# Optimization experiments

Hardware: AMD Instinct MI355X
Metric: run time of the kernel (lower is better)

Reference implementation:

```python
import jax, jax.numpy as jnp
import numpy as np

D_MODEL = 1024
NUM_HEADS = 16
D_IN = 1024

def setup_inputs() -> dict:
    key = jax.random.key(0)
    ks = jax.random.split(key, 5)
    scale = 1.0 / np.sqrt(D_IN)
    return {
        "in_features": jax.random.normal(ks[0], (4, 2048, D_IN), dtype=jnp.float32),
        "q_weight": jax.random.normal(ks[1], (D_MODEL, D_IN), dtype=jnp.float32) * scale,
        "k_weight": jax.random.normal(ks[2], (D_MODEL, D_IN), dtype=jnp.float32) * scale,
        "v_weight": jax.random.normal(ks[3], (D_MODEL, D_IN), dtype=jnp.float32) * scale,
        "o_weight": jax.random.normal(ks[4], (D_MODEL, D_MODEL), dtype=jnp.float32) * scale,
    }

def reference(in_features, q_weight, k_weight, v_weight, o_weight):
    batch, seq_len, _ = in_features.shape
    d_head = D_MODEL // NUM_HEADS
    # QKV projections (Linear with no bias: x @ W^T)
    q = jnp.einsum('bsi,di->bsd', in_features, q_weight)
    k = jnp.einsum('bsi,di->bsd', in_features, k_weight)
    v = jnp.einsum('bsi,di->bsd', in_features, v_weight)
    # split heads -> [b, h, s, d_head]
    q = q.reshape(batch, seq_len, NUM_HEADS, d_head).transpose(0, 2, 1, 3)
    k = k.reshape(batch, seq_len, NUM_HEADS, d_head).transpose(0, 2, 1, 3)
    v = v.reshape(batch, seq_len, NUM_HEADS, d_head).transpose(0, 2, 1, 3)
    # scaled dot-product attention (scale by per-head dim, as in SelfAttention)
    scores = jnp.einsum('bhqd,bhkd->bhqk', q, k) / jnp.sqrt(jnp.float32(d_head))
    probs = jax.nn.softmax(scores, axis=-1)
    ctx = jnp.einsum('bhqk,bhkd->bhqd', probs, v)
    # merge heads -> [b, s, d_model]
    ctx = ctx.transpose(0, 2, 1, 3).reshape(batch, seq_len, D_MODEL)
    # output projection
    return jnp.einsum('bsd,md->bsm', ctx, o_weight)
```

## Files before the change

kernel.cpp:

```cpp
#include <hip/hip_runtime.h>

typedef _Float16 half8 __attribute__((ext_vector_type(8)));
typedef _Float16 half4v __attribute__((ext_vector_type(4)));
typedef __fp16 fp16x2 __attribute__((ext_vector_type(2)));
typedef float f32x4 __attribute__((ext_vector_type(4)));
typedef float f32x16 __attribute__((ext_vector_type(16)));

__device__ __forceinline__ void gload_lds16(const _Float16* g, _Float16* l) {
    __builtin_amdgcn_global_load_lds(
        (const __attribute__((address_space(1))) void*)g,
        (__attribute__((address_space(3))) void*)l,
        16, 0, 0);
}

__global__ void cvt4_f32_f16(const float* __restrict__ s0, const float* __restrict__ s1,
                             const float* __restrict__ s2, const float* __restrict__ s3,
                             _Float16* __restrict__ dst) {
    int i = blockIdx.x * blockDim.x + threadIdx.x;
    int wsel = blockIdx.y;
    const float* src = (wsel == 0) ? s0 : (wsel == 1) ? s1 : (wsel == 2) ? s2 : s3;
    f32x4 v = ((const f32x4*)src)[i];
    half4v h;
    h[0] = (_Float16)v[0]; h[1] = (_Float16)v[1];
    h[2] = (_Float16)v[2]; h[3] = (_Float16)v[3];
    ((half4v*)(dst + (size_t)wsel * 1048576))[i] = h;
}

__global__ __launch_bounds__(256, 2)
void gemm_qkv(const float* __restrict__ X,
              const _Float16* __restrict__ Wbase,
              _Float16* __restrict__ outbase)
{
    __shared__ _Float16 As[2][4096];
    __shared__ _Float16 Bs[2][4096];

    const int tid  = threadIdx.x;
    const int lane = tid & 63;
    const int w    = tid >> 6;
    const int wr   = w >> 1, wc = w & 1;
    const int lr   = lane & 15, lg = lane >> 4;
    const int brow = blockIdx.x * 128;
    const int bcol = blockIdx.y * 128;
    const int mat  = blockIdx.z;

    const float*    Ap = X + (size_t)brow * 1024;
    const _Float16* Bp = Wbase + (size_t)mat * (1024u * 1024u) + (size_t)bcol * 1024;

    const int srw = tid >> 2;
    const int sch = tid & 3;
    const int rsw = (srw >> 1) & 3;
    const int bso = ((sch ^ rsw) << 3);
    const int aw0 = srw * 32        + ((sch ^ rsw) << 3);
    const int aw1 = (64 + srw) * 32 + ((sch ^ rsw) << 3);

    auto stageB = [&](int buf, int kt) {
        gload_lds16(Bp + (size_t)srw * 1024 + kt * 32 + bso,        &Bs[buf][w * 512]);
        gload_lds16(Bp + (size_t)(64 + srw) * 1024 + kt * 32 + bso, &Bs[buf][2048 + w * 512]);
    };

    f32x4 pa0, pa1, pa2, pa3;
    auto loadA = [&](int kt) {
        const float* p0 = Ap + (size_t)srw * 1024 + kt * 32 + sch * 8;
        const float* p1 = Ap + (size_t)(64 + srw) * 1024 + kt * 32 + sch * 8;
        pa0 = *(const f32x4*)p0;  pa1 = *(const f32x4*)(p0 + 4);
        pa2 = *(const f32x4*)p1;  pa3 = *(const f32x4*)(p1 + 4);
    };
    auto writeA = [&](int buf) {
        half8 h0, h1;
#pragma unroll
        for (int e = 0; e < 4; ++e) {
            h0[e]     = (_Float16)pa0[e];
            h0[4 + e] = (_Float16)pa1[e];
            h1[e]     = (_Float16)pa2[e];
            h1[4 + e] = (_Float16)pa3[e];
        }
        *(half8*)&As[buf][aw0] = h0;
        *(half8*)&As[buf][aw1] = h1;
    };

    f32x4 acc[4][4] = {};
    const int swz = ((lg ^ ((lr >> 1) & 3)) << 3);

    loadA(0);
    stageB(0, 0);
    writeA(0);
    loadA(1);
    __syncthreads();

    for (int t = 0; t < 32; ++t) {
        const int cur = t & 1;
        if (t < 31) {
            writeA(cur ^ 1);
            stageB(cur ^ 1, t + 1);
        }
        if (t < 30) loadA(t + 2);
        half8 af[4], bf[4];
#pragma unroll
        for (int mi = 0; mi < 4; ++mi)
            af[mi] = *(const half8*)&As[cur][(wr * 64 + mi * 16 + lr) * 32 + swz];
#pragma unroll
        for (int ni = 0; ni < 4; ++ni)
            bf[ni] = *(const half8*)&Bs[cur][(wc * 64 + ni * 16 + lr) * 32 + swz];
        __builtin_amdgcn_s_setprio(1);
#pragma unroll
        for (int mi = 0; mi < 4; ++mi)
#pragma unroll
            for (int ni = 0; ni < 4; ++ni)
                acc[mi][ni] = __builtin_amdgcn_mfma_f32_16x16x32_f16(af[mi], bf[ni], acc[mi][ni], 0, 0, 0);
        __builtin_amdgcn_s_setprio(0);
        __syncthreads();
    }

    _Float16* outp = outbase + (size_t)mat * (8192u * 1024u);
    if (mat == 2) {
        _Float16* Ts = &As[0][0];
#pragma unroll
        for (int p = 0; p < 2; ++p) {
            __syncthreads();
            if (wc == p) {
#pragma unroll
                for (int mi = 0; mi < 4; ++mi)
#pragma unroll
                    for (int ni = 0; ni < 4; ++ni) {
                        int drow = ni * 16 + lr;
                        int s0   = wr * 64 + mi * 16 + lg * 4;
                        half4v o;
#pragma unroll
                        for (int r = 0; r < 4; ++r) o[r] = (_Float16)acc[mi][ni][r];
                        int byteoff = drow * 256 + s0 * 2;
                        byteoff ^= (drow & 7) << 4;
                        *(half4v*)((char*)Ts + byteoff) = o;
                    }
            }
            __syncthreads();
            {
                int row   = tid >> 2;
                int cbase = (tid & 3) * 4;
                int gd = bcol + p * 64 + row;
                int h = gd >> 6, dd = gd & 63;
                int b = brow >> 11, sseq = brow & 2047;
                _Float16* gout = outp + (((size_t)b * 16 + h) * 64 + dd) * 2048 + sseq;
#pragma unroll
                for (int j = 0; j < 4; ++j) {
                    int c  = cbase + j;
                    int lc = c ^ (row & 7);
                    half8 v = *(const half8*)&Ts[row * 128 + lc * 8];
                    *(half8*)&gout[c * 8] = v;
                }
            }
        }
    } else {
        const float scale = (mat == 0) ? 0.18033688f : 1.0f;
#pragma unroll
        for (int mi = 0; mi < 4; ++mi)
#pragma unroll
            for (int ni = 0; ni < 4; ++ni)
#pragma unroll
                for (int r = 0; r < 4; ++r) {
                    int row = brow + wr * 64 + mi * 16 + lg * 4 + r;
                    int col = bcol + wc * 64 + ni * 16 + lr;
                    int b = row >> 11, s = row & 2047;
                    int h = col >> 6,  d = col & 63;
                    outp[(((size_t)b * 16 + h) * 2048 + s) * 64 + d] =
                        (_Float16)(acc[mi][ni][r] * scale);
                }
    }
}

__global__ __launch_bounds__(256, 2)
void gemm_o(const _Float16* __restrict__ A,
            const _Float16* __restrict__ Wbase,
            float* __restrict__ outp)
{
    __shared__ _Float16 lds[32768];
    _Float16* Asb = lds;
    _Float16* Bsb = lds + 16384;

    const int tid  = threadIdx.x;
    const int lane = tid & 63;
    const int w    = tid >> 6;
    const int wr   = w >> 1, wc = w & 1;
    const int lr   = lane & 15, lg = lane >> 4;
    const int brow = blockIdx.x * 128;
    const int bcol = blockIdx.y * 128;

    const _Float16* Ap = A + (size_t)brow * 1024;
    const _Float16* Bp = Wbase + (size_t)bcol * 1024;

    const int srw  = tid >> 2;
    const int sch  = tid & 3;
    const int soff = ((sch ^ ((srw >> 1) & 3)) << 3);

    auto stage = [&](int buf, int kt) {
#pragma unroll
        for (int i = 0; i < 2; ++i) {
            const int ra = i * 64 + srw;
            gload_lds16(Ap + (size_t)ra * 1024 + kt * 32 + soff,
                        Asb + buf * 4096 + i * 2048 + w * 512);
            gload_lds16(Bp + (size_t)ra * 1024 + kt * 32 + soff,
                        Bsb + buf * 4096 + i * 2048 + w * 512);
        }
    };

    f32x4 acc[4][4] = {};
    const int swz = ((lg ^ ((lr >> 1) & 3)) << 3);

    stage(0, 0);
    stage(1, 1);
    asm volatile("s_waitcnt vmcnt(4)" ::: "memory");
    __builtin_amdgcn_s_barrier();
    __builtin_amdgcn_sched_barrier(0);

    for (int t = 0; t < 32; ++t) {
        if (t < 30) stage((t + 2) & 3, t + 2);
        const _Float16* Ab = Asb + (t & 3) * 4096;
        const _Float16* Bb = Bsb + (t & 3) * 4096;
        half8 af[4], bf[4];
#pragma unroll
        for (int mi = 0; mi < 4; ++mi)
            af[mi] = *(const half8*)&Ab[(wr * 64 + mi * 16 + lr) * 32 + swz];
#pragma unroll
        for (int ni = 0; ni < 4; ++ni)
            bf[ni] = *(const half8*)&Bb[(wc * 64 + ni * 16 + lr) * 32 + swz];
        __builtin_amdgcn_s_setprio(1);
#pragma unroll
        for (int mi = 0; mi < 4; ++mi)
#pragma unroll
            for (int ni = 0; ni < 4; ++ni)
                acc[mi][ni] = __builtin_amdgcn_mfma_f32_16x16x32_f16(af[mi], bf[ni], acc[mi][ni], 0, 0, 0);
        __builtin_amdgcn_s_setprio(0);
        if (t < 30)       { asm volatile("s_waitcnt vmcnt(4)" ::: "memory"); }
        else if (t == 30) { asm volatile("s_waitcnt vmcnt(0)" ::: "memory"); }
        if (t < 31) {
            __builtin_amdgcn_s_barrier();
            __builtin_amdgcn_sched_barrier(0);
        }
    }

#pragma unroll
    for (int mi = 0; mi < 4; ++mi)
#pragma unroll
        for (int ni = 0; ni < 4; ++ni)
#pragma unroll
            for (int r = 0; r < 4; ++r) {
                int row = brow + wr * 64 + mi * 16 + lg * 4 + r;
                int col = bcol + wc * 64 + ni * 16 + lr;
                outp[(size_t)row * 1024 + col] = acc[mi][ni][r];
            }
}

#define M_FIX 10.0f
__global__ __launch_bounds__(256, 4)
void attn_kernel(const _Float16* __restrict__ Q,
                 const _Float16* __restrict__ Kx,
                 const _Float16* __restrict__ Vt,
                 _Float16* __restrict__ Ctx)
{
    __shared__ _Float16 Ks[2][64 * 72];
    __shared__ _Float16 Vs[2][64 * 72];

    const int tid = threadIdx.x, lane = tid & 63, w = tid >> 6;
    const int l31 = lane & 31, hi = lane >> 5;

    const int wg = blockIdx.x;
    const int j = ((wg & 7) << 7) + (wg >> 3);
    const int bh = j >> 4, qblk = j & 15;

    const _Float16* Qp  = Q  + ((size_t)bh * 2048 + qblk * 128) * 64;
    const _Float16* Kp  = Kx + (size_t)bh * 2048 * 64;
    const _Float16* Vtp = Vt + (size_t)bh * 64 * 2048;

    half8 qf[4];
#pragma unroll
    for (int ks = 0; ks < 4; ++ks)
        qf[ks] = *(const half8*)(Qp + (size_t)(w * 32 + l31) * 64 + ks * 16 + hi * 8);

    const int srow = tid >> 3;
    const int scol = (tid & 7) * 8;
    const _Float16* Kg0 = Kp  + (size_t)srow * 64   + scol;
    const _Float16* Vg0 = Vtp + (size_t)srow * 2048 + scol;
    const int ldso = srow * 72 + scol;

    const fp16x2 ones2 = {(__fp16)1.0f, (__fp16)1.0f};

    f32x16 cacc[2] = {};
    float l0 = 0.f, l1 = 0.f;

    half8 kr0, kr1, vr0, vr1;
    kr0 = *(const half8*)(Kg0);
    kr1 = *(const half8*)(Kg0 + 2048);
    vr0 = *(const half8*)(Vg0);
    vr1 = *(const half8*)(Vg0 + 32 * 2048);
    *(half8*)&Ks[0][ldso]           = kr0;
    *(half8*)&Ks[0][ldso + 32 * 72] = kr1;
    *(half8*)&Vs[0][ldso]           = vr0;
    *(half8*)&Vs[0][ldso + 32 * 72] = vr1;
    __syncthreads();

    for (int t = 0; t < 32; ++t) {
        const int cur = t & 1;
        if (t < 31) {
            kr0 = *(const half8*)(Kg0 + (size_t)(t + 1) * 4096);
            kr1 = *(const half8*)(Kg0 + (size_t)(t + 1) * 4096 + 2048);
        }

        f32x16 sf[2];
        __builtin_amdgcn_s_setprio(1);
#pragma unroll
        for (int kt = 0; kt < 2; ++kt) {
            f32x16 z;
#pragma unroll
            for (int r = 0; r < 16; ++r) z[r] = -M_FIX;
#pragma unroll
            for (int ks = 0; ks < 4; ++ks) {
                half8 kf = *(const half8*)&Ks[cur][(kt * 32 + l31) * 72 + ks * 16 + hi * 8];
                z = __builtin_amdgcn_mfma_f32_32x32x16_f16(kf, qf[ks], z, 0, 0, 0);
            }
            sf[kt] = z;
        }
        __builtin_amdgcn_s_setprio(0);

        if (t < 31) {
            *(half8*)&Ks[cur ^ 1][ldso]           = kr0;
            *(half8*)&Ks[cur ^ 1][ldso + 32 * 72] = kr1;
            vr0 = *(const half8*)(Vg0 + (t + 1) * 64);
            vr1 = *(const half8*)(Vg0 + (t + 1) * 64 + 32 * 2048);
        }

        half8 bf[4];
#pragma unroll
        for (int kt = 0; kt < 2; ++kt) {
#pragma unroll
            for (int r = 0; r < 16; ++r)
                sf[kt][r] = __builtin_amdgcn_exp2f(sf[kt][r]);

            unsigned uq[4][2];
#pragma unroll
            for (int qd = 0; qd < 4; ++qd)
#pragma unroll
                for (int w2 = 0; w2 < 2; ++w2)
                    uq[qd][w2] = __builtin_bit_cast(unsigned,
                        __builtin_amdgcn_cvt_pkrtz(sf[kt][4 * qd + 2 * w2],
                                                   sf[kt][4 * qd + 2 * w2 + 1]));

#pragma unroll
            for (int k1 = 0; k1 < 2; ++k1) {
                union { half8 h; unsigned u[4]; } bu;
#pragma unroll
                for (int w2 = 0; w2 < 2; ++w2) {
                    unsigned a = uq[2 * k1][w2];
                    unsigned b = uq[2 * k1 + 1][w2];
                    asm("v_permlane32_swap_b32 %0, %1" : "+v"(a), "+v"(b));
                    bu.u[w2]     = a;
                    bu.u[2 + w2] = b;
                }
                l0 = __builtin_amdgcn_fdot2(__builtin_bit_cast(fp16x2, bu.u[0]), ones2, l0, false);
                l1 = __builtin_amdgcn_fdot2(__builtin_bit_cast(fp16x2, bu.u[1]), ones2, l1, false);
                l0 = __builtin_amdgcn_fdot2(__builtin_bit_cast(fp16x2, bu.u[2]), ones2, l0, false);
                l1 = __builtin_amdgcn_fdot2(__builtin_bit_cast(fp16x2, bu.u[3]), ones2, l1, false);
                bf[kt * 2 + k1] = bu.h;
            }
        }

        __builtin_amdgcn_s_setprio(1);
#pragma unroll
        for (int dt = 0; dt < 2; ++dt)
#pragma unroll
            for (int ks = 0; ks < 4; ++ks) {
                half8 vf = *(const half8*)&Vs[cur][(dt * 32 + l31) * 72 + ks * 16 + hi * 8];
                cacc[dt] = __builtin_amdgcn_mfma_f32_32x32x16_f16(vf, bf[ks], cacc[dt], 0, 0, 0);
            }
        __builtin_amdgcn_s_setprio(0);

        if (t < 31) {
            *(half8*)&Vs[cur ^ 1][ldso]           = vr0;
            *(half8*)&Vs[cur ^ 1][ldso + 32 * 72] = vr1;
        }
        __syncthreads();
    }

    float l = l0 + l1;
    const float inv = 1.0f / (l + __shfl_xor(l, 32, 64));
    const int s = qblk * 128 + w * 32 + l31;
    _Float16* Cp = Ctx + ((size_t)(bh >> 4) * 2048 + s) * 1024 + (bh & 15) * 64;
#pragma unroll
    for (int dt = 0; dt < 2; ++dt)
#pragma unroll
        for (int qd = 0; qd < 4; ++qd) {
            half4v o;
#pragma unroll
            for (int j2 = 0; j2 < 4; ++j2) o[j2] = (_Float16)(cacc[dt][4 * qd + j2] * inv);
            *(half4v*)&Cp[dt * 32 + qd * 8 + hi * 4] = o;
        }
}

extern "C" void kernel_launch(void* const* d_in, const int* in_sizes, int n_in,
                              void* d_out, int out_size, void* d_ws, size_t ws_size,
                              hipStream_t stream)
{
    const float* X  = (const float*)d_in[0];
    const float* Wq = (const float*)d_in[1];
    const float* Wk = (const float*)d_in[2];
    const float* Wv = (const float*)d_in[3];
    const float* Wo = (const float*)d_in[4];

    if (ws_size < (size_t)(8 + 4 + 24) * 1024 * 1024 * 2) return;
    _Float16* Ctx = (_Float16*)d_ws;
    _Float16* Wh  = Ctx + (size_t)8 * 1024 * 1024;
    _Float16* QKV = Wh + (size_t)4 * 1024 * 1024;

    cvt4_f32_f16<<<dim3(1024, 4), 256, 0, stream>>>(Wq, Wk, Wv, Wo, Wh);

    gemm_qkv<<<dim3(64, 8, 3), 256, 0, stream>>>(X, Wh, QKV);

    attn_kernel<<<1024, 256, 0, stream>>>(QKV, QKV + 8388608, QKV + 16777216, Ctx);

    gemm_o<<<dim3(64, 8), 256, 0, stream>>>(Ctx, Wh + 3145728, (float*)d_out);
}
```

Measured before the change: 191.1 us.

## Stage attention K/V tiles via direct global-to-LDS loads with XOR swizzle

Replaces the register-staged K/V prefetch (global load into registers, then LDS store) in the attention kernel with buffer global_load_lds 16-byte direct copies into a double-buffered LDS tile. The padded 72-stride layout becomes an unpadded 64-stride layout with an XOR chunk swizzle to avoid bank conflicts on the MFMA fragment reads. This frees VGPRs and removes the explicit LDS store instructions. It relies on the single per-iteration barrier to cover completion of the asynchronous LDS writes, and the swizzle must match the per-wave contiguous destination layout.

```diff
diff --git a/kernel.cpp b/kernel.cpp
--- a/kernel.cpp
+++ b/kernel.cpp
@@ -256,8 +256,8 @@
                  const _Float16* __restrict__ Vt,
                  _Float16* __restrict__ Ctx)
 {
-    __shared__ _Float16 Ks[2][64 * 72];
-    __shared__ _Float16 Vs[2][64 * 72];
+    __shared__ _Float16 Ks[2][4096];
+    __shared__ _Float16 Vs[2][4096];
 
     const int tid = threadIdx.x, lane = tid & 63, w = tid >> 6;
     const int l31 = lane & 31, hi = lane >> 5;
@@ -276,33 +276,29 @@
         qf[ks] = *(const half8*)(Qp + (size_t)(w * 32 + l31) * 64 + ks * 16 + hi * 8);
 
     const int srow = tid >> 3;
-    const int scol = (tid & 7) * 8;
-    const _Float16* Kg0 = Kp  + (size_t)srow * 64   + scol;
-    const _Float16* Vg0 = Vtp + (size_t)srow * 2048 + scol;
-    const int ldso = srow * 72 + scol;
+    const int schk = (tid & 7) ^ ((srow >> 2) & 7);
+    const _Float16* Kst = Kp  + (size_t)srow * 64   + schk * 8;
+    const _Float16* Vst = Vtp + (size_t)srow * 2048 + schk * 8;
+
+    auto stageKV = [&](int buf, int t) {
+        gload_lds16(Kst + (size_t)t * 4096,         &Ks[buf][w * 512]);
+        gload_lds16(Kst + (size_t)t * 4096 + 2048,  &Ks[buf][2048 + w * 512]);
+        gload_lds16(Vst + t * 64,                   &Vs[buf][w * 512]);
+        gload_lds16(Vst + t * 64 + 32 * 2048,       &Vs[buf][2048 + w * 512]);
+    };
 
     const fp16x2 ones2 = {(__fp16)1.0f, (__fp16)1.0f};
+    const int rsw2 = (l31 >> 2) << 3;
 
     f32x16 cacc[2] = {};
     float l0 = 0.f, l1 = 0.f;
 
-    half8 kr0, kr1, vr0, vr1;
-    kr0 = *(const half8*)(Kg0);
-    kr1 = *(const half8*)(Kg0 + 2048);
-    vr0 = *(const half8*)(Vg0);
-    vr1 = *(const half8*)(Vg0 + 32 * 2048);
-    *(half8*)&Ks[0][ldso]           = kr0;
-    *(half8*)&Ks[0][ldso + 32 * 72] = kr1;
-    *(half8*)&Vs[0][ldso]           = vr0;
-    *(half8*)&Vs[0][ldso + 32 * 72] = vr1;
+    stageKV(0, 0);
     __syncthreads();
 
     for (int t = 0; t < 32; ++t) {
         const int cur = t & 1;
-        if (t < 31) {
-            kr0 = *(const half8*)(Kg0 + (size_t)(t + 1) * 4096);
-            kr1 = *(const half8*)(Kg0 + (size_t)(t + 1) * 4096 + 2048);
-        }
+        if (t < 31) stageKV(cur ^ 1, t + 1);
 
         f32x16 sf[2];
         __builtin_amdgcn_s_setprio(1);
@@ -313,19 +309,12 @@
             for (int r = 0; r < 16; ++r) z[r] = -M_FIX;
 #pragma unroll
             for (int ks = 0; ks < 4; ++ks) {
-                half8 kf = *(const half8*)&Ks[cur][(kt * 32 + l31) * 72 + ks * 16 + hi * 8];
+                half8 kf = *(const half8*)&Ks[cur][(kt * 32 + l31) * 64 + ((ks * 16 + hi * 8) ^ rsw2)];
                 z = __builtin_amdgcn_mfma_f32_32x32x16_f16(kf, qf[ks], z, 0, 0, 0);
             }
             sf[kt] = z;
         }
         __builtin_amdgcn_s_setprio(0);
-
-        if (t < 31) {
-            *(half8*)&Ks[cur ^ 1][ldso]           = kr0;
-            *(half8*)&Ks[cur ^ 1][ldso + 32 * 72] = kr1;
-            vr0 = *(const half8*)(Vg0 + (t + 1) * 64);
-            vr1 = *(const half8*)(Vg0 + (t + 1) * 64 + 32 * 2048);
-        }
 
         half8 bf[4];
 #pragma unroll
@@ -367,15 +356,11 @@
         for (int dt = 0; dt < 2; ++dt)
 #pragma unroll
             for (int ks = 0; ks < 4; ++ks) {
-                half8 vf = *(const half8*)&Vs[cur][(dt * 32 + l31) * 72 + ks * 16 + hi * 8];
+                half8 vf = *(const half8*)&Vs[cur][(dt * 32 + l31) * 64 + ((ks * 16 + hi * 8) ^ rsw2)];
                 cacc[dt] = __builtin_amdgcn_mfma_f32_32x32x16_f16(vf, bf[ks], cacc[dt], 0, 0, 0);
             }
         __builtin_amdgcn_s_setprio(0);
 
-        if (t < 31) {
-            *(half8*)&Vs[cur ^ 1][ldso]           = vr0;
-            *(half8*)&Vs[cur ^ 1][ldso + 32 * 72] = vr1;
-        }
         __syncthreads();
     }
 
```

Result: no change. 190.2 us (-0.5%).
